# Kernel optimization log

Hardware: AMD Instinct MI355X
Metric: run time of the kernel (lower is better)

Reference implementation:

```python
import jax, jax.numpy as jnp
import numpy as np

B, L, E, H = 2, 2048, 1024, 16
HD = E // H          # head_dim = 64
G = H // 4           # heads per kernel-size group = 4


def _dwconv(x, w, b):
    """Causal depthwise conv. x: (B, G, L, D); w: (D, k); b: (D,).
    Matches PadLeft(k-1) + Conv1d(D, D, k, groups=D): y[l] = sum_j w[:, j] * x[l - (k-1) + j] + b."""
    k = w.shape[-1]
    Lx = x.shape[2]
    xp = jnp.pad(x, ((0, 0), (0, 0), (k - 1, 0), (0, 0)))
    out = b
    for j in range(k):
        out = out + xp[:, :, j:j + Lx, :] * w[:, j]
    return out


def setup_inputs() -> dict:
    key = jax.random.key(0)
    ks = jax.random.split(key, 32)
    s = 0.02
    inp = {"x": jax.random.normal(ks[0], (B, L, E), jnp.float32)}
    for i, n in enumerate(["Wq", "Wk", "Wv", "Wo"]):
        inp[n] = jax.random.normal(ks[1 + i], (E, E), jnp.float32) * s
    inp["bo"] = jax.random.normal(ks[5], (E,), jnp.float32) * s
    i = 6
    for ksz in (3, 5, 7):
        for pfx in ("q", "k", "v"):
            inp[f"{pfx}{ksz}_w"] = jax.random.normal(ks[i], (HD, ksz), jnp.float32) * (1.0 / ksz)
            inp[f"{pfx}{ksz}_b"] = jax.random.normal(ks[i + 1], (HD,), jnp.float32) * s
            i += 2
    return inp


def reference(x, Wq, Wk, Wv, Wo, bo,
              q3_w, q3_b, k3_w, k3_b, v3_w, v3_b,
              q5_w, q5_b, k5_w, k5_b, v5_w, v5_b,
              q7_w, q7_b, k7_w, k7_b, v7_w, v7_b):
    b, l, _ = x.shape

    def split(t):  # (b, l, E) -> (b, 4, G, l, HD)
        return t.reshape(b, l, 4, G, HD).transpose(0, 2, 3, 1, 4)

    q = split(x @ Wq.T)
    k = split(x @ Wk.T)
    v = split(x @ Wv.T)

    # NOTE: faithful to source quirks -- k and v convs are applied to the
    # (already convolved) q group, not to k/v.
    q0, k0, v0 = q[:, 0], k[:, 0], v[:, 0]
    q1 = _dwconv(q[:, 1], q3_w, q3_b)
    k1 = _dwconv(q1, k3_w, k3_b)
    v1 = _dwconv(q1, v3_w, v3_b)
    q2 = _dwconv(q[:, 2], q5_w, q5_b)
    k2 = _dwconv(q2, k5_w, k5_b)
    v2 = _dwconv(q2, v5_w, v5_b)
    q3 = _dwconv(q[:, 3], q7_w, q7_b)
    k3 = _dwconv(q3, k7_w, k7_b)
    v3 = _dwconv(q3, v7_w, v7_b)

    Q = jnp.concatenate([q0, q1, q2, q3], axis=1)  # (b, H, l, HD)
    K = jnp.concatenate([k0, k1, k2, k3], axis=1)
    V = jnp.concatenate([v0, v1, v2, v3], axis=1)

    logit = jnp.einsum('bnid,bnjd->bnij', Q, K) * (HD ** -0.5)
    attn = jax.nn.softmax(logit, axis=-1)
    attn_out = jnp.einsum('bnij,bnjd->bnid', attn, V)

    # Source quirk: output uses rearranged V, discarding attn_out.
    out = V.transpose(0, 2, 1, 3).reshape(b, l, E)
    # keep the attention compute alive without changing the math
    out = out + 0.0 * attn_out.transpose(0, 2, 1, 3).reshape(b, l, E)
    return out @ Wo.T + bo
```

## Files before the change

### kernel.cpp

```cpp
#include <hip/hip_runtime.h>
#include <hip/hip_bf16.h>
#include <stdint.h>

#define L_SEQ 2048
#define MTOT  4096
#define EDIM  1024

typedef __attribute__((ext_vector_type(8))) short bf16x8;
typedef __attribute__((ext_vector_type(4))) float f32x4;
typedef __attribute__((ext_vector_type(4))) float float4v;
typedef __attribute__((ext_vector_type(4))) unsigned short us4;
typedef __attribute__((ext_vector_type(2))) unsigned int u32x2;

__device__ __forceinline__ unsigned short f2b(float f) {
    union { float f; unsigned u; } v; v.f = f;
    return (unsigned short)((v.u + 0x7FFFu + ((v.u >> 16) & 1u)) >> 16);
}
__device__ __forceinline__ float b2f(unsigned short h) {
    union { unsigned u; float f; } v; v.u = ((unsigned)h) << 16;
    return v.f;
}

__device__ __forceinline__ void lds16(const void* g, void* l) {
    __builtin_amdgcn_global_load_lds((const __attribute__((address_space(1))) void*)g,
                                     (__attribute__((address_space(3))) void*)l, 16, 0, 0);
}

__global__ __launch_bounds__(256) void prep_kernel(
    const float* __restrict__ x, const float* __restrict__ Wq,
    const float* __restrict__ Wv, const float* __restrict__ Wo,
    unsigned short* __restrict__ xb, unsigned short* __restrict__ W1b,
    unsigned short* __restrict__ Wob,
    const float* __restrict__ q3w, const float* __restrict__ q3b,
    const float* __restrict__ v3w, const float* __restrict__ v3b,
    const float* __restrict__ q5w, const float* __restrict__ q5b,
    const float* __restrict__ v5w, const float* __restrict__ v5b,
    const float* __restrict__ q7w, const float* __restrict__ q7b,
    const float* __restrict__ v7w, const float* __restrict__ v7b,
    float* __restrict__ H, float* __restrict__ Beff, float* __restrict__ Corr)
{
    const int XQ = (MTOT * EDIM) / 4;
    const int WQ = (EDIM * EDIM) / 4;
    if (blockIdx.x >= 6144) {
        int ch = (blockIdx.x - 6144) * 256 + threadIdx.x;
        int g = ch >> 8;
        int d = ch & 63;
        int k = 3 + 2 * g;
        const float* qw = (g == 0) ? q3w : (g == 1) ? q5w : q7w;
        const float* qb = (g == 0) ? q3b : (g == 1) ? q5b : q7b;
        const float* vw = (g == 0) ? v3w : (g == 1) ? v5w : v7w;
        const float* vb = (g == 0) ? v3b : (g == 1) ? v5b : v7b;

        float hq[7], hv[7];
        for (int i = 0; i < 7; ++i) { hq[i] = 0.f; hv[i] = 0.f; }
        for (int i = 0; i < k; ++i) {
            hq[i] = qw[d * k + (k - 1 - i)];
            hv[i] = vw[d * k + (k - 1 - i)];
        }
        float h[13];
        for (int i = 0; i < 13; ++i) h[i] = 0.f;
        for (int a = 0; a < 7; ++a)
            for (int b = 0; b < 7; ++b)
                h[a + b] += hq[a] * hv[b];
        for (int i = 0; i < 13; ++i) H[i * 768 + ch] = h[i];

        float sv = 0.f;
        for (int j = 0; j < k; ++j) sv += vw[d * k + j];
        Beff[ch] = qb[d] * sv + vb[d];

        for (int l = 0; l < 6; ++l) {
            float s2 = 0.f;
            for (int i = l + 1; i < 7; ++i) s2 += hv[i];
            Corr[l * 768 + ch] = qb[d] * s2;
        }
        return;
    }
    int i = blockIdx.x * 256 + threadIdx.x;
    const float* src;
    unsigned short* dst;
    int j;
    if (i < XQ) {
        j = i * 4; src = x; dst = xb;
    } else if (i < XQ + WQ) {
        j = (i - XQ) * 4;
        int row = j >> 10;
        src = (row < 256) ? Wv : Wq;
        dst = W1b;
    } else {
        j = (i - XQ - WQ) * 4; src = Wo; dst = Wob;
    }
    float4v v = *(const float4v*)(src + j);
    us4 o;
    o[0] = f2b(v[0]); o[1] = f2b(v[1]); o[2] = f2b(v[2]); o[3] = f2b(v[3]);
    *(us4*)(dst + j) = o;
}

template <int OUT_MODE>
__global__ __launch_bounds__(512, 4) void gemm_pipe(
    const unsigned short* __restrict__ A, const unsigned short* __restrict__ BT,
    unsigned short* __restrict__ Cb, float* __restrict__ Cf,
    const float* __restrict__ bias, int M, int N, int K)
{
    __shared__ unsigned short As[3][128 * 64];
    __shared__ unsigned short Bs[3][64 * 64];

    const int nbx = N >> 6;
    int orig = blockIdx.y * nbx + blockIdx.x;
    int nwg  = (M >> 7) * nbx;
    int wg   = (orig & 7) * (nwg >> 3) + (orig >> 3);
    const int m0 = (wg / nbx) * 128, n0 = (wg % nbx) * 64;

    const int tid  = threadIdx.x;
    const int wid  = tid >> 6;
    const int lane = tid & 63;
    const int wr   = wid >> 1, wc = wid & 1;
    const int fr   = lane & 15, fq = lane >> 4;

    f32x4 acc[2][2] = {};

    const unsigned short* Aptr = A  + (size_t)m0 * K;
    const unsigned short* Bptr = BT + (size_t)n0 * K;

    const int cA1 = 512 + tid;
    const size_t offA0 = (size_t)(tid >> 3) * K + (((tid & 7) ^ ((tid >> 3) & 7)) * 8);
    const size_t offA1 = (size_t)(cA1 >> 3) * K + (((cA1 & 7) ^ ((cA1 >> 3) & 7)) * 8);
    const size_t offB  = offA0;

    auto stage = [&](int buf, int t) {
        const unsigned short* Ab = Aptr + (t << 6);
        const unsigned short* Bb = Bptr + (t << 6);
        lds16(Ab + offA0, &As[buf][(wid * 64) * 8]);
        lds16(Ab + offA1, &As[buf][(512 + wid * 64) * 8]);
        lds16(Bb + offB,  &Bs[buf][(wid * 64) * 8]);
    };

    auto compute = [&](int buf) {
        const unsigned short* as = As[buf];
        const unsigned short* bs = Bs[buf];
#pragma unroll
        for (int s = 0; s < 2; ++s) {
            bf16x8 a[2], b[2];
#pragma unroll
            for (int mi = 0; mi < 2; ++mi) {
                int row = wr * 32 + mi * 16 + fr;
                a[mi] = *(const bf16x8*)(as + row * 64 + (((s * 4 + fq) ^ (row & 7)) * 8));
            }
#pragma unroll
            for (int ni = 0; ni < 2; ++ni) {
                int row = wc * 32 + ni * 16 + fr;
                b[ni] = *(const bf16x8*)(bs + row * 64 + (((s * 4 + fq) ^ (row & 7)) * 8));
            }
#pragma unroll
            for (int mi = 0; mi < 2; ++mi)
#pragma unroll
                for (int ni = 0; ni < 2; ++ni)
                    acc[mi][ni] = __builtin_amdgcn_mfma_f32_16x16x32_bf16(a[mi], b[ni], acc[mi][ni], 0, 0, 0);
        }
    };

    const int NT = K >> 6;
    stage(0, 0);
    stage(1, 1);
    asm volatile("s_waitcnt vmcnt(3)" ::: "memory");
    __builtin_amdgcn_s_barrier();
    asm volatile("" ::: "memory");

    for (int t = 0; t < NT; ++t) {
        if (t + 2 < NT) stage((t + 2) % 3, t + 2);
        compute(t % 3);
        if (t + 1 < NT) {
            if (t + 2 < NT) {
                asm volatile("s_waitcnt vmcnt(3)" ::: "memory");
            } else {
                asm volatile("s_waitcnt vmcnt(0)" ::: "memory");
            }
            __builtin_amdgcn_s_barrier();
            asm volatile("" ::: "memory");
        }
    }

#pragma unroll
    for (int mi = 0; mi < 2; ++mi) {
#pragma unroll
        for (int ni = 0; ni < 2; ++ni) {
            int col  = n0 + wc * 32 + ni * 16 + fr;
            int rowb = m0 + wr * 32 + mi * 16 + fq * 4;
#pragma unroll
            for (int j = 0; j < 4; ++j) {
                float v = acc[mi][ni][j];
                if (OUT_MODE == 0) {
                    Cb[(size_t)(rowb + j) * N + col] = f2b(v);
                } else {
                    Cf[(size_t)(rowb + j) * N + col] = v + bias[col];
                }
            }
        }
    }
}

__global__ __launch_bounds__(256) void conv_kernel(
    const unsigned short* __restrict__ T, unsigned short* __restrict__ V,
    const float* __restrict__ H, const float* __restrict__ Beff,
    const float* __restrict__ Corr)
{
    int w  = blockIdx.x * 256 + threadIdx.x;
    int m  = (w >> 8) * 2;
    int e0 = (w & 255) * 4;
    const unsigned short* tp = T + (size_t)m * EDIM + e0;
    unsigned short*       vp = V + (size_t)m * EDIM + e0;
    if (e0 < 256) {
        *(u32x2*)vp = *(const u32x2*)tp;
        *(u32x2*)(vp + EDIM) = *(const u32x2*)(tp + EDIM);
        return;
    }
    int l  = m & (L_SEQ - 1);
    int ch = e0 - 256;
    float4v b4 = *(const float4v*)(Beff + ch);
    float4v acc0 = b4, acc1 = b4;

    {
        float4v h = *(const float4v*)(H + ch);
        us4 t = *(const us4*)(tp + EDIM);
        acc1[0] += h[0] * b2f(t[0]); acc1[1] += h[1] * b2f(t[1]);
        acc1[2] += h[2] * b2f(t[2]); acc1[3] += h[3] * b2f(t[3]);
    }
    int ni = (l < 12) ? l : 12;
    for (int i = 0; i <= ni; ++i) {
        us4 t = *(const us4*)(tp - (size_t)i * EDIM);
        float4v h0 = *(const float4v*)(H + i * 768 + ch);
        acc0[0] += h0[0] * b2f(t[0]); acc0[1] += h0[1] * b2f(t[1]);
        acc0[2] += h0[2] * b2f(t[2]); acc0[3] += h0[3] * b2f(t[3]);
        if (i < 12) {
            float4v h1 = *(const float4v*)(H + (i + 1) * 768 + ch);
            acc1[0] += h1[0] * b2f(t[0]); acc1[1] += h1[1] * b2f(t[1]);
            acc1[2] += h1[2] * b2f(t[2]); acc1[3] += h1[3] * b2f(t[3]);
        }
    }
    if (l < 6) {
        float4v c = *(const float4v*)(Corr + l * 768 + ch);
        acc0[0] -= c[0]; acc0[1] -= c[1]; acc0[2] -= c[2]; acc0[3] -= c[3];
    }
    if (l + 1 < 6) {
        float4v c = *(const float4v*)(Corr + (l + 1) * 768 + ch);
        acc1[0] -= c[0]; acc1[1] -= c[1]; acc1[2] -= c[2]; acc1[3] -= c[3];
    }
    us4 o0, o1;
    o0[0] = f2b(acc0[0]); o0[1] = f2b(acc0[1]); o0[2] = f2b(acc0[2]); o0[3] = f2b(acc0[3]);
    o1[0] = f2b(acc1[0]); o1[1] = f2b(acc1[1]); o1[2] = f2b(acc1[2]); o1[3] = f2b(acc1[3]);
    *(us4*)vp = o0;
    *(us4*)(vp + EDIM) = o1;
}

extern "C" void kernel_launch(void* const* d_in, const int* in_sizes, int n_in,
                              void* d_out, int out_size, void* d_ws, size_t ws_size,
                              hipStream_t stream)
{
    const float* x  = (const float*)d_in[0];
    const float* Wq = (const float*)d_in[1];
    const float* Wv = (const float*)d_in[3];
    const float* Wo = (const float*)d_in[4];
    const float* bo = (const float*)d_in[5];

    uint8_t* ws = (uint8_t*)d_ws;
    unsigned short* xb  = (unsigned short*)(ws);
    unsigned short* W1b = (unsigned short*)(ws + (8u  << 20));
    unsigned short* Wob = (unsigned short*)(ws + (10u << 20));
    unsigned short* T   = (unsigned short*)(ws + (12u << 20));
    unsigned short* V   = (unsigned short*)(ws + (20u << 20));
    float* H    = (float*)(ws + (28u << 20));
    float* Beff = (float*)(ws + (28u << 20) + (64u << 10));
    float* Corr = (float*)(ws + (28u << 20) + (96u << 10));

    prep_kernel<<<6147, 256, 0, stream>>>(
        x, Wq, Wv, Wo, xb, W1b, Wob,
        (const float*)d_in[6],  (const float*)d_in[7],
        (const float*)d_in[10], (const float*)d_in[11],
        (const float*)d_in[12], (const float*)d_in[13],
        (const float*)d_in[16], (const float*)d_in[17],
        (const float*)d_in[18], (const float*)d_in[19],
        (const float*)d_in[22], (const float*)d_in[23],
        H, Beff, Corr);

    dim3 gg(EDIM / 64, MTOT / 128);
    gemm_pipe<0><<<gg, 512, 0, stream>>>(xb, W1b, T, nullptr, nullptr, MTOT, EDIM, EDIM);

    conv_kernel<<<2048, 256, 0, stream>>>(T, V, H, Beff, Corr);

    gemm_pipe<1><<<gg, 512, 0, stream>>>(V, Wob, nullptr, (float*)d_out, bo, MTOT, EDIM, EDIM);
}
```

Baseline: 57.72 us.

## Use 128x128 GEMM tiles with intra-block split-K across wave pairs

Doubles the GEMM output tile to 128x128 and splits each 64-wide K slice between two wave groups. The partial accumulators are reduced through LDS before the epilogue. The aim is more operand reuse per LDS load and fewer LDS reads per MFMA. The cost is half as many workgroups, higher register pressure from the 4x4 accumulators, and an extra LDS reduction step.

```diff
diff --git a/kernel.cpp b/kernel.cpp
--- a/kernel.cpp
+++ b/kernel.cpp
@@ -96,72 +96,71 @@
 }
 
 template <int OUT_MODE>
-__global__ __launch_bounds__(512, 4) void gemm_pipe(
+__global__ __launch_bounds__(512, 2) void gemm_ks(
     const unsigned short* __restrict__ A, const unsigned short* __restrict__ BT,
     unsigned short* __restrict__ Cb, float* __restrict__ Cf,
     const float* __restrict__ bias, int M, int N, int K)
 {
-    __shared__ unsigned short As[3][128 * 64];
-    __shared__ unsigned short Bs[3][64 * 64];
-
-    const int nbx = N >> 6;
+    __shared__ unsigned short sh[3 * 16384];
+
+    const int nbx = N >> 7;
     int orig = blockIdx.y * nbx + blockIdx.x;
     int nwg  = (M >> 7) * nbx;
     int wg   = (orig & 7) * (nwg >> 3) + (orig >> 3);
-    const int m0 = (wg / nbx) * 128, n0 = (wg % nbx) * 64;
+    const int m0 = (wg / nbx) * 128, n0 = (wg % nbx) * 128;
 
     const int tid  = threadIdx.x;
     const int wid  = tid >> 6;
     const int lane = tid & 63;
-    const int wr   = wid >> 1, wc = wid & 1;
+    const int wr   = wid >> 2;
+    const int wc   = (wid >> 1) & 1;
+    const int kh   = wid & 1;
     const int fr   = lane & 15, fq = lane >> 4;
 
-    f32x4 acc[2][2] = {};
+    f32x4 acc[4][4] = {};
 
     const unsigned short* Aptr = A  + (size_t)m0 * K;
     const unsigned short* Bptr = BT + (size_t)n0 * K;
 
-    const int cA1 = 512 + tid;
     const size_t offA0 = (size_t)(tid >> 3) * K + (((tid & 7) ^ ((tid >> 3) & 7)) * 8);
-    const size_t offA1 = (size_t)(cA1 >> 3) * K + (((cA1 & 7) ^ ((cA1 >> 3) & 7)) * 8);
-    const size_t offB  = offA0;
+    const size_t offA1 = offA0 + (size_t)64 * K;
 
     auto stage = [&](int buf, int t) {
-        const unsigned short* Ab = Aptr + (t << 6);
-        const unsigned short* Bb = Bptr + (t << 6);
-        lds16(Ab + offA0, &As[buf][(wid * 64) * 8]);
-        lds16(Ab + offA1, &As[buf][(512 + wid * 64) * 8]);
-        lds16(Bb + offB,  &Bs[buf][(wid * 64) * 8]);
+        unsigned short* Al = sh + buf * 16384;
+        unsigned short* Bl = Al + 8192;
+        const unsigned short* Ag = Aptr + (t << 6);
+        const unsigned short* Bg = Bptr + (t << 6);
+        lds16(Ag + offA0, Al + tid * 8);
+        lds16(Ag + offA1, Al + (512 + tid) * 8);
+        lds16(Bg + offA0, Bl + tid * 8);
+        lds16(Bg + offA1, Bl + (512 + tid) * 8);
     };
 
     auto compute = [&](int buf) {
-        const unsigned short* as = As[buf];
-        const unsigned short* bs = Bs[buf];
-#pragma unroll
-        for (int s = 0; s < 2; ++s) {
-            bf16x8 a[2], b[2];
-#pragma unroll
-            for (int mi = 0; mi < 2; ++mi) {
-                int row = wr * 32 + mi * 16 + fr;
-                a[mi] = *(const bf16x8*)(as + row * 64 + (((s * 4 + fq) ^ (row & 7)) * 8));
-            }
-#pragma unroll
-            for (int ni = 0; ni < 2; ++ni) {
-                int row = wc * 32 + ni * 16 + fr;
-                b[ni] = *(const bf16x8*)(bs + row * 64 + (((s * 4 + fq) ^ (row & 7)) * 8));
-            }
-#pragma unroll
-            for (int mi = 0; mi < 2; ++mi)
-#pragma unroll
-                for (int ni = 0; ni < 2; ++ni)
-                    acc[mi][ni] = __builtin_amdgcn_mfma_f32_16x16x32_bf16(a[mi], b[ni], acc[mi][ni], 0, 0, 0);
-        }
+        const unsigned short* as = sh + buf * 16384;
+        const unsigned short* bs = as + 8192;
+        bf16x8 a[4], b[4];
+#pragma unroll
+        for (int mi = 0; mi < 4; ++mi) {
+            int row = wr * 64 + mi * 16 + fr;
+            a[mi] = *(const bf16x8*)(as + row * 64 + (((kh * 4 + fq) ^ (row & 7)) * 8));
+        }
+#pragma unroll
+        for (int ni = 0; ni < 4; ++ni) {
+            int row = wc * 64 + ni * 16 + fr;
+            b[ni] = *(const bf16x8*)(bs + row * 64 + (((kh * 4 + fq) ^ (row & 7)) * 8));
+        }
+#pragma unroll
+        for (int mi = 0; mi < 4; ++mi)
+#pragma unroll
+            for (int ni = 0; ni < 4; ++ni)
+                acc[mi][ni] = __builtin_amdgcn_mfma_f32_16x16x32_bf16(a[mi], b[ni], acc[mi][ni], 0, 0, 0);
     };
 
     const int NT = K >> 6;
     stage(0, 0);
     stage(1, 1);
-    asm volatile("s_waitcnt vmcnt(3)" ::: "memory");
+    asm volatile("s_waitcnt vmcnt(4)" ::: "memory");
     __builtin_amdgcn_s_barrier();
     asm volatile("" ::: "memory");
 
@@ -170,7 +169,7 @@
         compute(t % 3);
         if (t + 1 < NT) {
             if (t + 2 < NT) {
-                asm volatile("s_waitcnt vmcnt(3)" ::: "memory");
+                asm volatile("s_waitcnt vmcnt(4)" ::: "memory");
             } else {
                 asm volatile("s_waitcnt vmcnt(0)" ::: "memory");
             }
@@ -179,19 +178,38 @@
         }
     }
 
-#pragma unroll
-    for (int mi = 0; mi < 2; ++mi) {
-#pragma unroll
-        for (int ni = 0; ni < 2; ++ni) {
-            int col  = n0 + wc * 32 + ni * 16 + fr;
-            int rowb = m0 + wr * 32 + mi * 16 + fq * 4;
-#pragma unroll
-            for (int j = 0; j < 4; ++j) {
-                float v = acc[mi][ni][j];
-                if (OUT_MODE == 0) {
-                    Cb[(size_t)(rowb + j) * N + col] = f2b(v);
-                } else {
-                    Cf[(size_t)(rowb + j) * N + col] = v + bias[col];
+    __syncthreads();
+    float* Mg = (float*)sh;
+    const int mgbase = (wr * 2 + wc) * 4096;
+    if (kh) {
+#pragma unroll
+        for (int mi = 0; mi < 4; ++mi)
+#pragma unroll
+            for (int ni = 0; ni < 4; ++ni) {
+                int col = ni * 16 + fr;
+                int adr = mgbase + col * 64 + (((mi * 4 + fq) ^ (col & 15)) << 2);
+                *(f32x4*)(Mg + adr) = acc[mi][ni];
+            }
+    }
+    __syncthreads();
+    if (!kh) {
+#pragma unroll
+        for (int mi = 0; mi < 4; ++mi) {
+#pragma unroll
+            for (int ni = 0; ni < 4; ++ni) {
+                int col = ni * 16 + fr;
+                int adr = mgbase + col * 64 + (((mi * 4 + fq) ^ (col & 15)) << 2);
+                f32x4 p = *(const f32x4*)(Mg + adr);
+                int gcol = n0 + wc * 64 + col;
+                int rowb = m0 + wr * 64 + mi * 16 + fq * 4;
+#pragma unroll
+                for (int j = 0; j < 4; ++j) {
+                    float v = acc[mi][ni][j] + p[j];
+                    if (OUT_MODE == 0) {
+                        Cb[(size_t)(rowb + j) * N + gcol] = f2b(v);
+                    } else {
+                        Cf[(size_t)(rowb + j) * N + gcol] = v + bias[gcol];
+                    }
                 }
             }
         }
@@ -281,10 +299,10 @@
         (const float*)d_in[22], (const float*)d_in[23],
         H, Beff, Corr);
 
-    dim3 gg(EDIM / 64, MTOT / 128);
-    gemm_pipe<0><<<gg, 512, 0, stream>>>(xb, W1b, T, nullptr, nullptr, MTOT, EDIM, EDIM);
+    dim3 gg(EDIM / 128, MTOT / 128);
+    gemm_ks<0><<<gg, 512, 0, stream>>>(xb, W1b, T, nullptr, nullptr, MTOT, EDIM, EDIM);
 
     conv_kernel<<<2048, 256, 0, stream>>>(T, V, H, Beff, Corr);
 
-    gemm_pipe<1><<<gg, 512, 0, stream>>>(V, Wob, nullptr, (float*)d_out, bo, MTOT, EDIM, EDIM);
-}
+    gemm_ks<1><<<gg, 512, 0, stream>>>(V, Wob, nullptr, (float*)d_out, bo, MTOT, EDIM, EDIM);
+}
```

Measured after the change: 55.61 us. -3.7%, faster.
